# Kernel optimization log

Measured on AMD Instinct MI355X. Metric: run time of the kernel, lower is better.

Reference implementation:

```python
import jax, jax.numpy as jnp
import numpy as np

D_HEAD = 64
SCALE = 1.0 / (D_HEAD ** 0.5)
MASK_VALUE = -1e9


def setup_inputs() -> dict:
    key = jax.random.key(0)
    kq, kk, kv, km = jax.random.split(key, 4)
    B, H, S, D = 2, 12, 2048, D_HEAD
    Q = jax.random.normal(kq, (B, H, S, D), dtype=jnp.float32)
    K = jax.random.normal(kk, (B, H, S, D), dtype=jnp.float32)
    V = jax.random.normal(kv, (B, H, S, D), dtype=jnp.float32)
    attn_mask = jax.random.randint(km, (B, 1, S, S), 0, 2).astype(bool)
    return {"Q": Q, "K": K, "V": V, "attn_mask": attn_mask}


def reference(Q, K, V, attn_mask):
    # scores: [B,H,S,S]
    scores = jnp.einsum('bhqd,bhkd->bhqk', Q, K) * SCALE
    scores = jnp.where(attn_mask, MASK_VALUE, scores)
    attn_prob = jax.nn.softmax(scores, axis=-1)
    # dropout p=0.0 (eval mode) -> identity
    context = jnp.einsum('bhqk,bhkd->bhqd', attn_prob, V)
    return (context, attn_prob)
```

## Files before the change

### kernel.cpp

```cpp
#include <hip/hip_runtime.h>
#include <hip/hip_bf16.h>
#include <math.h>

#define B_SZ   2
#define NH     12
#define S_LEN  2048
#define D_HD   64
#define NQ_EL  ((size_t)B_SZ * NH * S_LEN * D_HD)

typedef __attribute__((ext_vector_type(8))) __bf16 bf16x8;
typedef __attribute__((ext_vector_type(4))) __bf16 bf16x4;
typedef __attribute__((ext_vector_type(4))) float  f32x4;
typedef __attribute__((ext_vector_type(4))) unsigned u32x4;

__device__ __forceinline__ int detect_mask_mode64(const void* mask) {
  const int lane = threadIdx.x & 63;
  unsigned v = ((const unsigned*)mask)[lane];
  if (__ballot(v <= 1u) == ~0ull) return 0;
  if (__ballot(v == 0u || v == 0x3f800000u) == ~0ull) return 2;
  unsigned h0 = v & 0xFFFFu, h1 = v >> 16;
  bool okb = (h0 == 0u || h0 == 0x3f80u) && (h1 == 0u || h1 == 0x3f80u);
  if (__ballot(okb) == ~0ull) return 3;
  return 1;
}

__device__ __forceinline__ bool mask_at(const void* mask, int mode, size_t idx) {
  if (mode == 0) return ((const int*)mask)[idx] != 0;
  if (mode == 1) return ((const unsigned char*)mask)[idx] != 0;
  if (mode == 2) return ((const float*)mask)[idx] != 0.0f;
  return ((const unsigned short*)mask)[idx] != 0;
}

__global__ __launch_bounds__(256)
void prep_kernel(const float* __restrict__ Q, const float* __restrict__ K,
                 const float* __restrict__ V, const void* __restrict__ mask,
                 unsigned* __restrict__ bits, __bf16* __restrict__ Qb,
                 __bf16* __restrict__ Kb, __bf16* __restrict__ VT) {
  const int blk = blockIdx.x;
  const int tid = threadIdx.x;
  if (blk < 512) {
    const int mode = detect_mask_mode64(mask);
    const int lane = tid & 63;
#pragma unroll 4
    for (int i = 0; i < 64; ++i) {
      const size_t idx = ((size_t)blk * 64 + i) * 256 + tid;
      const unsigned long long bal = __ballot(mask_at(mask, mode, idx));
      if (lane == 0)       bits[idx >> 5] = (unsigned)bal;
      else if (lane == 32) bits[idx >> 5] = (unsigned)(bal >> 32);
    }
  } else if (blk < 1536) {
    const bool isq = blk < 1024;
    const float* src = isq ? Q : K;
    __bf16* dst = isq ? Qb : Kb;
    const float scale = isq ? 0.125f : 1.0f;
    const size_t base = (size_t)(blk & 511) * 256 + tid;
#pragma unroll
    for (int i = 0; i < 6; ++i) {
      const size_t li = base + (size_t)i * 512 * 256;
      float4 a = ((const float4*)src)[li];
      __bf16 o0 = (__bf16)(a.x * scale), o1 = (__bf16)(a.y * scale);
      __bf16 o2 = (__bf16)(a.z * scale), o3 = (__bf16)(a.w * scale);
      ((ushort4*)dst)[li] = (ushort4){
          __builtin_bit_cast(unsigned short, o0), __builtin_bit_cast(unsigned short, o1),
          __builtin_bit_cast(unsigned short, o2), __builtin_bit_cast(unsigned short, o3)};
    }
  } else {
    __shared__ __align__(16) __bf16 tl[D_HD][72];
    const int t  = blk - 1536;
    const int bh = t >> 5;
    const int k0 = (t & 31) * 64;
#pragma unroll
    for (int i = 0; i < 4; ++i) {
      const int vi = i * 256 + tid;
      const int kk = vi >> 4, dv = (vi & 15) * 4;
      float4 f = *(const float4*)(V + ((size_t)bh * S_LEN + k0 + kk) * D_HD + dv);
      tl[dv + 0][kk] = (__bf16)f.x; tl[dv + 1][kk] = (__bf16)f.y;
      tl[dv + 2][kk] = (__bf16)f.z; tl[dv + 3][kk] = (__bf16)f.w;
    }
    __syncthreads();
#pragma unroll
    for (int half = 0; half < 2; ++half) {
      const int d = half * 32 + (tid >> 3);
      const int kc = (tid & 7) * 8;
      bf16x8 vv = *(const bf16x8*)&tl[d][kc];
      *(bf16x8*)(VT + ((size_t)bh * D_HD + d) * S_LEN + k0 + kc) = vv;
    }
  }
}

__device__ __forceinline__ bf16x8 ld8f(const float* p, float scale) {
  const float4 a = *(const float4*)p;
  const float4 b = *(const float4*)(p + 4);
  bf16x8 r;
  r[0] = (__bf16)(a.x * scale); r[1] = (__bf16)(a.y * scale);
  r[2] = (__bf16)(a.z * scale); r[3] = (__bf16)(a.w * scale);
  r[4] = (__bf16)(b.x * scale); r[5] = (__bf16)(b.y * scale);
  r[6] = (__bf16)(b.z * scale); r[7] = (__bf16)(b.w * scale);
  return r;
}

__device__ __forceinline__ float bflo(unsigned u) {
  return __builtin_bit_cast(float, u << 16);
}
__device__ __forceinline__ float bfhi(unsigned u) {
  return __builtin_bit_cast(float, u & 0xFFFF0000u);
}

__global__ __launch_bounds__(512, 4)
void attn_main(const __bf16* __restrict__ Qb, const __bf16* __restrict__ Kb,
               const __bf16* __restrict__ VT, const unsigned* __restrict__ mbits,
               float* __restrict__ out_ctx)
{
  float* out_p = out_ctx + NQ_EL;

  const int flat = blockIdx.x + blockIdx.y * gridDim.x;
  const int wf   = (flat & 7) * 384 + (flat >> 3);
  const int bh   = wf >> 7;
  const int qg   = wf & 127;
  const int b    = bh / NH;

  const int tid  = threadIdx.x;
  const int lane = tid & 63;
  const int w    = tid >> 6;
  const int qbase = qg * 16;
  const int col  = lane & 15;
  const int g    = lane >> 4;
  const int q    = qbase + col;
  const int k0   = w * 256;

  const size_t mbase = ((size_t)b * S_LEN + q) * (S_LEN / 32);
  const size_t khead = (size_t)bh * S_LEN;

  const size_t qoff = (khead + q) * D_HD + g * 8;
  const bf16x8 bq0 = *(const bf16x8*)(Qb + qoff);
  const bf16x8 bq1 = *(const bf16x8*)(Qb + qoff + 32);

  __shared__ float lsh[8][16];
  __shared__ float linv_s[16];
  __shared__ float csum[8][16][66];

  unsigned pe[8][4];
  float lsum = 0.f;

  bf16x8 nk0a, nk0b, nk1a, nk1b;
  {
    const size_t koff0 = (khead + k0 + col) * D_HD + g * 8;
    const size_t koff1 = (khead + k0 + 16 + col) * D_HD + g * 8;
    nk0a = *(const bf16x8*)(Kb + koff0);
    nk0b = *(const bf16x8*)(Kb + koff0 + 32);
    nk1a = *(const bf16x8*)(Kb + koff1);
    nk1b = *(const bf16x8*)(Kb + koff1 + 32);
  }
  unsigned nmw = mbits[mbase + (k0 >> 5)];

#pragma unroll
  for (int c = 0; c < 8; ++c) {
    const bf16x8 k0a = nk0a, k0b = nk0b, k1a = nk1a, k1b = nk1b;
    const unsigned mw = nmw;
    if (c < 7) {
      const int kn = k0 + (c + 1) * 32;
      const size_t koff0 = (khead + kn + col) * D_HD + g * 8;
      const size_t koff1 = (khead + kn + 16 + col) * D_HD + g * 8;
      nk0a = *(const bf16x8*)(Kb + koff0);
      nk0b = *(const bf16x8*)(Kb + koff0 + 32);
      nk1a = *(const bf16x8*)(Kb + koff1);
      nk1b = *(const bf16x8*)(Kb + koff1 + 32);
      nmw = mbits[mbase + (kn >> 5)];
    }
    float e[8];
    {
      f32x4 acc = {0.f, 0.f, 0.f, 0.f};
      acc = __builtin_amdgcn_mfma_f32_16x16x32_bf16(k0a, bq0, acc, 0, 0, 0);
      acc = __builtin_amdgcn_mfma_f32_16x16x32_bf16(k0b, bq1, acc, 0, 0, 0);
#pragma unroll
      for (int r = 0; r < 4; ++r) {
        const bool msk = (mw >> (g * 4 + r)) & 1;
        e[r] = msk ? 0.f : __expf(acc[r]);
        lsum += e[r];
      }
    }
    {
      f32x4 acc = {0.f, 0.f, 0.f, 0.f};
      acc = __builtin_amdgcn_mfma_f32_16x16x32_bf16(k1a, bq0, acc, 0, 0, 0);
      acc = __builtin_amdgcn_mfma_f32_16x16x32_bf16(k1b, bq1, acc, 0, 0, 0);
#pragma unroll
      for (int r = 0; r < 4; ++r) {
        const bool msk = (mw >> (16 + g * 4 + r)) & 1;
        e[4 + r] = msk ? 0.f : __expf(acc[r]);
        lsum += e[4 + r];
      }
    }
#pragma unroll
    for (int j = 0; j < 4; ++j) {
      unsigned lo = __builtin_bit_cast(unsigned short, (__bf16)e[2 * j]);
      unsigned hi = __builtin_bit_cast(unsigned short, (__bf16)e[2 * j + 1]);
      pe[c][j] = (hi << 16) | lo;
    }
  }
  lsum += __shfl_xor(lsum, 16);
  lsum += __shfl_xor(lsum, 32);
  if (lane < 16) lsh[w][col] = lsum;
  __syncthreads();
  {
    float tot = 0.f;
#pragma unroll
    for (int w8 = 0; w8 < 8; ++w8) tot += lsh[w8][col];
    if (w == 0 && lane < 16) linv_s[col] = 1.0f / tot;
  }
  const int Lr = lane >> 3;
  const int u  = lane & 7;
  float linv_t[2];
#pragma unroll
  for (int t = 0; t < 2; ++t) {
    float tot = 0.f;
#pragma unroll
    for (int w8 = 0; w8 < 8; ++w8) tot += lsh[w8][t * 8 + Lr];
    linv_t[t] = 1.0f / tot;
  }
  const int subg = u >> 2;

  f32x4 cacc[4];
#pragma unroll
  for (int dt = 0; dt < 4; dt++) cacc[dt] = (f32x4){0.f, 0.f, 0.f, 0.f};

  float* pblk = out_p + (size_t)bh * S_LEN * S_LEN + (size_t)qbase * S_LEN + k0;
  const __bf16* vbase = VT + (size_t)bh * D_HD * S_LEN;

#pragma unroll
  for (int c = 0; c < 8; ++c) {
    const int kc = k0 + c * 32;
    bf16x8 vf[4];
#pragma unroll
    for (int dt = 0; dt < 4; dt++) {
      const __bf16* vrow = vbase + (size_t)(dt * 16 + col) * S_LEN + kc;
      bf16x4 lo = *(const bf16x4*)(vrow + g * 4);
      bf16x4 hi = *(const bf16x4*)(vrow + 16 + g * 4);
      vf[dt] = __builtin_shufflevector(lo, hi, 0, 1, 2, 3, 4, 5, 6, 7);
    }
#pragma unroll
    for (int t = 0; t < 2; ++t) {
      const int src = 16 * (u & 3) + t * 8 + Lr;
      unsigned a0 = (unsigned)__shfl((int)pe[c][0], src);
      unsigned a1 = (unsigned)__shfl((int)pe[c][1], src);
      unsigned a2 = (unsigned)__shfl((int)pe[c][2], src);
      unsigned a3 = (unsigned)__shfl((int)pe[c][3], src);
      const unsigned lo = subg ? a2 : a0;
      const unsigned hi = subg ? a3 : a1;
      const float lv = linv_t[t];
      f32x4 st = {bflo(lo) * lv, bfhi(lo) * lv, bflo(hi) * lv, bfhi(hi) * lv};
      __builtin_nontemporal_store(
          st, (f32x4*)(pblk + (size_t)(t * 8 + Lr) * S_LEN + c * 32 + u * 4));
    }
    u32x4 w4 = {pe[c][0], pe[c][1], pe[c][2], pe[c][3]};
    bf16x8 pa = __builtin_bit_cast(bf16x8, w4);
#pragma unroll
    for (int dt = 0; dt < 4; dt++)
      cacc[dt] = __builtin_amdgcn_mfma_f32_16x16x32_bf16(pa, vf[dt], cacc[dt], 0, 0, 0);
  }

#pragma unroll
  for (int dt = 0; dt < 4; dt++)
#pragma unroll
    for (int r = 0; r < 4; r++)
      csum[w][g * 4 + r][dt * 16 + col] = cacc[dt][r];
  __syncthreads();
  {
    const int qo = tid >> 5;
    const int d0 = (tid * 2) & 63;
    float s0 = 0.f, s1 = 0.f;
#pragma unroll
    for (int w8 = 0; w8 < 8; ++w8) {
      s0 += csum[w8][qo][d0];
      s1 += csum[w8][qo][d0 + 1];
    }
    const float lv = linv_s[qo];
    float2 o = {s0 * lv, s1 * lv};
    *(float2*)(out_ctx + ((size_t)bh * S_LEN + qbase + qo) * D_HD + d0) = o;
  }
}

template<bool USE_BITS>
__global__ __launch_bounds__(512)
void attn_fb(const float* __restrict__ Qg, const float* __restrict__ Kg,
             const float* __restrict__ Vg, const void* __restrict__ mask,
             const unsigned* __restrict__ mbits, float* __restrict__ out_ctx)
{
  float* out_p = out_ctx + NQ_EL;
  const int flat = blockIdx.x + blockIdx.y * gridDim.x;
  const int wf   = (flat & 7) * 96 + (flat >> 3);
  const int qt = wf & 31, bh = wf >> 5, b = bh / NH;
  const int tid = threadIdx.x, lane = tid & 63, w = tid >> 6;
  const int qw = w & 3, kh = w >> 2;
  const int qbase = qt * 64 + qw * 16;
  const int col = lane & 15, g = lane >> 4;
  const int q = qbase + col;
  const int k0 = kh * (S_LEN / 2);
  int mmode = 0;
  if constexpr (!USE_BITS) mmode = detect_mask_mode64(mask);
  const size_t mrow  = (size_t)b * S_LEN * S_LEN;
  const size_t mbase = ((size_t)b * S_LEN + q) * (S_LEN / 32);
  const size_t qoff = ((size_t)bh * S_LEN + q) * D_HD + g * 8;
  const bf16x8 bq0 = ld8f(Qg + qoff, 0.125f);
  const bf16x8 bq1 = ld8f(Qg + qoff + 32, 0.125f);

  float lsum = 0.f;
  for (int kc = k0; kc < k0 + S_LEN / 2; kc += 32) {
    unsigned mw = 0;
    if constexpr (USE_BITS) mw = mbits[mbase + (kc >> 5)];
#pragma unroll
    for (int sub = 0; sub < 2; ++sub) {
      const int kb = kc + sub * 16;
      const size_t koff = ((size_t)bh * S_LEN + kb + col) * D_HD + g * 8;
      bf16x8 ak0 = ld8f(Kg + koff, 1.0f);
      bf16x8 ak1 = ld8f(Kg + koff + 32, 1.0f);
      f32x4 acc = {0.f, 0.f, 0.f, 0.f};
      acc = __builtin_amdgcn_mfma_f32_16x16x32_bf16(ak0, bq0, acc, 0, 0, 0);
      acc = __builtin_amdgcn_mfma_f32_16x16x32_bf16(ak1, bq1, acc, 0, 0, 0);
#pragma unroll
      for (int r = 0; r < 4; ++r) {
        bool msk;
        if constexpr (USE_BITS) msk = (mw >> (sub * 16 + g * 4 + r)) & 1;
        else msk = mask_at(mask, mmode, mrow + (size_t)q * S_LEN + kb + g * 4 + r);
        lsum += msk ? 0.f : __expf(acc[r]);
      }
    }
  }
  lsum += __shfl_xor(lsum, 16);
  lsum += __shfl_xor(lsum, 32);
  __shared__ float lsh[8][16];
  __shared__ float csum[4][16][66];
  if (lane < 16) lsh[w][col] = lsum;
  __syncthreads();
  const float inv_l = 1.0f / (lsum + lsh[w ^ 4][col]);

  f32x4 cacc[4];
#pragma unroll
  for (int dt = 0; dt < 4; dt++) cacc[dt] = (f32x4){0.f, 0.f, 0.f, 0.f};
  float* prow = out_p + (size_t)bh * S_LEN * S_LEN + (size_t)q * S_LEN;

  for (int it = 0; it < S_LEN / 64; ++it) {
    const int kc = k0 + it * 32;
    unsigned mw = 0;
    if constexpr (USE_BITS) mw = mbits[mbase + (kc >> 5)];
    float p[8];
#pragma unroll
    for (int sub = 0; sub < 2; ++sub) {
      const int kb = kc + sub * 16;
      const size_t koff = ((size_t)bh * S_LEN + kb + col) * D_HD + g * 8;
      bf16x8 ak0 = ld8f(Kg + koff, 1.0f);
      bf16x8 ak1 = ld8f(Kg + koff + 32, 1.0f);
      f32x4 acc = {0.f, 0.f, 0.f, 0.f};
      acc = __builtin_amdgcn_mfma_f32_16x16x32_bf16(ak0, bq0, acc, 0, 0, 0);
      acc = __builtin_amdgcn_mfma_f32_16x16x32_bf16(ak1, bq1, acc, 0, 0, 0);
#pragma unroll
      for (int r = 0; r < 4; ++r) {
        bool msk;
        if constexpr (USE_BITS) msk = (mw >> (sub * 16 + g * 4 + r)) & 1;
        else msk = mask_at(mask, mmode, mrow + (size_t)q * S_LEN + kb + g * 4 + r);
        p[sub * 4 + r] = msk ? 0.f : __expf(acc[r]) * inv_l;
      }
      float4 st = {p[sub * 4 + 0], p[sub * 4 + 1], p[sub * 4 + 2], p[sub * 4 + 3]};
      *(float4*)(prow + kb + g * 4) = st;
    }
    bf16x8 pa;
#pragma unroll
    for (int e = 0; e < 8; e++) pa[e] = (__bf16)p[e];
#pragma unroll
    for (int dt = 0; dt < 4; dt++) {
      bf16x8 vf;
#pragma unroll
      for (int e = 0; e < 8; e++) {
        const int kidx = kc + (e >> 2) * 16 + g * 4 + (e & 3);
        vf[e] = (__bf16)Vg[((size_t)bh * S_LEN + kidx) * D_HD + dt * 16 + col];
      }
      cacc[dt] = __builtin_amdgcn_mfma_f32_16x16x32_bf16(pa, vf, cacc[dt], 0, 0, 0);
    }
  }
  if (kh == 1) {
#pragma unroll
    for (int dt = 0; dt < 4; dt++)
#pragma unroll
      for (int r = 0; r < 4; r++)
        csum[qw][g * 4 + r][dt * 16 + col] = cacc[dt][r];
  }
  __syncthreads();
  if (kh == 0) {
#pragma unroll
    for (int dt = 0; dt < 4; dt++)
#pragma unroll
      for (int r = 0; r < 4; r++)
        out_ctx[((size_t)bh * S_LEN + qbase + g * 4 + r) * D_HD + dt * 16 + col] =
            cacc[dt][r] + csum[qw][g * 4 + r][dt * 16 + col];
  }
}

__global__ __launch_bounds__(256)
void build_bits_kernel(const void* __restrict__ mask, unsigned* __restrict__ bits) {
  const int mode = detect_mask_mode64(mask);
  const size_t i = (size_t)blockIdx.x * 256 + threadIdx.x;
  const unsigned long long bal = __ballot(mask_at(mask, mode, i));
  const int lane = threadIdx.x & 63;
  if (lane == 0)       bits[i >> 5] = (unsigned)bal;
  else if (lane == 32) bits[i >> 5] = (unsigned)(bal >> 32);
}

extern "C" void kernel_launch(void* const* d_in, const int* in_sizes, int n_in,
                              void* d_out, int out_size, void* d_ws, size_t ws_size,
                              hipStream_t stream) {
  const float* Q = (const float*)d_in[0];
  const float* K = (const float*)d_in[1];
  const float* V = (const float*)d_in[2];
  const void* mask = d_in[3];
  float* out = (float*)d_out;

  const size_t mask_elems = (size_t)B_SZ * S_LEN * S_LEN;
  const size_t off_bits = 256;
  const size_t off_q  = off_bits + mask_elems / 8;
  const size_t off_k  = off_q + NQ_EL * 2;
  const size_t off_vt = off_k + NQ_EL * 2;
  const size_t need   = off_vt + NQ_EL * 2;

  if (ws_size >= need) {
    unsigned* bits = (unsigned*)((char*)d_ws + off_bits);
    __bf16* Qb = (__bf16*)((char*)d_ws + off_q);
    __bf16* Kb = (__bf16*)((char*)d_ws + off_k);
    __bf16* VT = (__bf16*)((char*)d_ws + off_vt);
    prep_kernel<<<2304, 256, 0, stream>>>(Q, K, V, mask, bits, Qb, Kb, VT);
    dim3 grid(128, 24);
    attn_main<<<grid, 512, 0, stream>>>(Qb, Kb, VT, bits, out);
  } else if (ws_size >= off_q) {
    unsigned* bits = (unsigned*)((char*)d_ws + off_bits);
    build_bits_kernel<<<(unsigned)(mask_elems / 256), 256, 0, stream>>>(mask, bits);
    dim3 gfb(S_LEN / 64, B_SZ * NH);
    attn_fb<true><<<gfb, 512, 0, stream>>>(Q, K, V, mask, bits, out);
  } else {
    dim3 gfb(S_LEN / 64, B_SZ * NH);
    attn_fb<false><<<gfb, 512, 0, stream>>>(Q, K, V, mask, nullptr, out);
  }
}
```

Measured before the change: 313.6 us.

## Split attention into compute pass and separate probability normalization kernel

The main attention kernel now writes unnormalized bf16 exponentials and per-row inverse sums to workspace, computes the context, and leaves probability output to a new streaming normalization kernel. The aim is to decouple the large fp32 probability write from the MFMA compute kernel and give it fully coalesced row-contiguous stores. This adds a large intermediate write and read through workspace, and it runs only when the workspace is big enough; otherwise the old monolithic kernel is used.

```diff
diff --git a/kernel.cpp b/kernel.cpp
--- a/kernel.cpp
+++ b/kernel.cpp
@@ -7,6 +7,7 @@
 #define S_LEN  2048
 #define D_HD   64
 #define NQ_EL  ((size_t)B_SZ * NH * S_LEN * D_HD)
+#define NROWS  ((size_t)B_SZ * NH * S_LEN)
 
 typedef __attribute__((ext_vector_type(8))) __bf16 bf16x8;
 typedef __attribute__((ext_vector_type(4))) __bf16 bf16x4;
@@ -107,12 +108,11 @@
 }
 
 __global__ __launch_bounds__(512, 4)
-void attn_main(const __bf16* __restrict__ Qb, const __bf16* __restrict__ Kb,
-               const __bf16* __restrict__ VT, const unsigned* __restrict__ mbits,
-               float* __restrict__ out_ctx)
+void attn_compute(const __bf16* __restrict__ Qb, const __bf16* __restrict__ Kb,
+                  const __bf16* __restrict__ VT, const unsigned* __restrict__ mbits,
+                  float* __restrict__ out_ctx, unsigned short* __restrict__ ebuf,
+                  float* __restrict__ linvg)
 {
-  float* out_p = out_ctx + NQ_EL;
-
   const int flat = blockIdx.x + blockIdx.y * gridDim.x;
   const int wf   = (flat & 7) * 384 + (flat >> 3);
   const int bh   = wf >> 7;
@@ -196,6 +196,14 @@
       unsigned hi = __builtin_bit_cast(unsigned short, (__bf16)e[2 * j + 1]);
       pe[c][j] = (hi << 16) | lo;
     }
+    const int kc = k0 + c * 32;
+    unsigned long long v01 = (unsigned long long)pe[c][0] |
+                             ((unsigned long long)pe[c][1] << 32);
+    unsigned long long v23 = (unsigned long long)pe[c][2] |
+                             ((unsigned long long)pe[c][3] << 32);
+    unsigned short* erow = ebuf + (khead + q) * S_LEN;
+    *(unsigned long long*)(erow + kc + g * 4)      = v01;
+    *(unsigned long long*)(erow + kc + 16 + g * 4) = v23;
   }
   lsum += __shfl_xor(lsum, 16);
   lsum += __shfl_xor(lsum, 32);
@@ -205,6 +213,142 @@
     float tot = 0.f;
 #pragma unroll
     for (int w8 = 0; w8 < 8; ++w8) tot += lsh[w8][col];
+    if (w == 0 && lane < 16) {
+      const float lv = 1.0f / tot;
+      linv_s[col] = lv;
+      linvg[khead + q] = lv;
+    }
+  }
+
+  f32x4 cacc[4];
+#pragma unroll
+  for (int dt = 0; dt < 4; dt++) cacc[dt] = (f32x4){0.f, 0.f, 0.f, 0.f};
+  const __bf16* vbase = VT + (size_t)bh * D_HD * S_LEN;
+
+#pragma unroll
+  for (int c = 0; c < 8; ++c) {
+    const int kc = k0 + c * 32;
+    u32x4 w4 = {pe[c][0], pe[c][1], pe[c][2], pe[c][3]};
+    bf16x8 pa = __builtin_bit_cast(bf16x8, w4);
+#pragma unroll
+    for (int dt = 0; dt < 4; dt++) {
+      const __bf16* vrow = vbase + (size_t)(dt * 16 + col) * S_LEN + kc;
+      bf16x4 lo = *(const bf16x4*)(vrow + g * 4);
+      bf16x4 hi = *(const bf16x4*)(vrow + 16 + g * 4);
+      bf16x8 vf = __builtin_shufflevector(lo, hi, 0, 1, 2, 3, 4, 5, 6, 7);
+      cacc[dt] = __builtin_amdgcn_mfma_f32_16x16x32_bf16(pa, vf, cacc[dt], 0, 0, 0);
+    }
+  }
+
+#pragma unroll
+  for (int dt = 0; dt < 4; dt++)
+#pragma unroll
+    for (int r = 0; r < 4; r++)
+      csum[w][g * 4 + r][dt * 16 + col] = cacc[dt][r];
+  __syncthreads();
+  {
+    const int qo = tid >> 5;
+    const int d0 = (tid * 2) & 63;
+    float s0 = 0.f, s1 = 0.f;
+#pragma unroll
+    for (int w8 = 0; w8 < 8; ++w8) {
+      s0 += csum[w8][qo][d0];
+      s1 += csum[w8][qo][d0 + 1];
+    }
+    const float lv = linv_s[qo];
+    float2 o = {s0 * lv, s1 * lv};
+    *(float2*)(out_ctx + ((size_t)bh * S_LEN + qbase + qo) * D_HD + d0) = o;
+  }
+}
+
+__global__ __launch_bounds__(256)
+void norm_kernel(const unsigned short* __restrict__ ebuf,
+                 const float* __restrict__ linvg, float* __restrict__ out_p)
+{
+  const int tid = threadIdx.x;
+#pragma unroll
+  for (int i = 0; i < 16; ++i) {
+    const size_t row = (size_t)blockIdx.x * 16 + i;
+    const float lv = linvg[row];
+    const unsigned short* erow = ebuf + row * S_LEN;
+    float* prow = out_p + row * S_LEN;
+#pragma unroll
+    for (int s = 0; s < 2; ++s) {
+      const int col = s * 1024 + tid * 4;
+      const unsigned long long v = *(const unsigned long long*)(erow + col);
+      const unsigned u0 = (unsigned)v, u1 = (unsigned)(v >> 32);
+      f32x4 st = {bflo(u0) * lv, bfhi(u0) * lv, bflo(u1) * lv, bfhi(u1) * lv};
+      *(f32x4*)(prow + col) = st;
+    }
+  }
+}
+
+__global__ __launch_bounds__(512, 4)
+void attn_mono(const __bf16* __restrict__ Qb, const __bf16* __restrict__ Kb,
+               const __bf16* __restrict__ VT, const unsigned* __restrict__ mbits,
+               float* __restrict__ out_ctx)
+{
+  float* out_p = out_ctx + NQ_EL;
+  const int flat = blockIdx.x + blockIdx.y * gridDim.x;
+  const int wf   = (flat & 7) * 384 + (flat >> 3);
+  const int bh   = wf >> 7;
+  const int qg   = wf & 127;
+  const int b    = bh / NH;
+  const int tid  = threadIdx.x;
+  const int lane = tid & 63;
+  const int w    = tid >> 6;
+  const int qbase = qg * 16;
+  const int col  = lane & 15;
+  const int g    = lane >> 4;
+  const int q    = qbase + col;
+  const int k0   = w * 256;
+  const size_t mbase = ((size_t)b * S_LEN + q) * (S_LEN / 32);
+  const size_t khead = (size_t)bh * S_LEN;
+  const size_t qoff = (khead + q) * D_HD + g * 8;
+  const bf16x8 bq0 = *(const bf16x8*)(Qb + qoff);
+  const bf16x8 bq1 = *(const bf16x8*)(Qb + qoff + 32);
+  __shared__ float lsh[8][16];
+  __shared__ float linv_s[16];
+  __shared__ float csum[8][16][66];
+  unsigned pe[8][4];
+  float lsum = 0.f;
+#pragma unroll
+  for (int c = 0; c < 8; ++c) {
+    const int kc = k0 + c * 32;
+    const unsigned mw = mbits[mbase + (kc >> 5)];
+    float e[8];
+#pragma unroll
+    for (int sub = 0; sub < 2; ++sub) {
+      const int kb = kc + sub * 16;
+      const size_t koff = (khead + kb + col) * D_HD + g * 8;
+      bf16x8 ak0 = *(const bf16x8*)(Kb + koff);
+      bf16x8 ak1 = *(const bf16x8*)(Kb + koff + 32);
+      f32x4 acc = {0.f, 0.f, 0.f, 0.f};
+      acc = __builtin_amdgcn_mfma_f32_16x16x32_bf16(ak0, bq0, acc, 0, 0, 0);
+      acc = __builtin_amdgcn_mfma_f32_16x16x32_bf16(ak1, bq1, acc, 0, 0, 0);
+#pragma unroll
+      for (int r = 0; r < 4; ++r) {
+        const bool msk = (mw >> (sub * 16 + g * 4 + r)) & 1;
+        float ev = msk ? 0.f : __expf(acc[r]);
+        e[sub * 4 + r] = ev;
+        lsum += ev;
+      }
+    }
+#pragma unroll
+    for (int j = 0; j < 4; ++j) {
+      unsigned lo = __builtin_bit_cast(unsigned short, (__bf16)e[2 * j]);
+      unsigned hi = __builtin_bit_cast(unsigned short, (__bf16)e[2 * j + 1]);
+      pe[c][j] = (hi << 16) | lo;
+    }
+  }
+  lsum += __shfl_xor(lsum, 16);
+  lsum += __shfl_xor(lsum, 32);
+  if (lane < 16) lsh[w][col] = lsum;
+  __syncthreads();
+  {
+    float tot = 0.f;
+#pragma unroll
+    for (int w8 = 0; w8 < 8; ++w8) tot += lsh[w8][col];
     if (w == 0 && lane < 16) linv_s[col] = 1.0f / tot;
   }
   const int Lr = lane >> 3;
@@ -218,14 +362,11 @@
     linv_t[t] = 1.0f / tot;
   }
   const int subg = u >> 2;
-
   f32x4 cacc[4];
 #pragma unroll
   for (int dt = 0; dt < 4; dt++) cacc[dt] = (f32x4){0.f, 0.f, 0.f, 0.f};
-
   float* pblk = out_p + (size_t)bh * S_LEN * S_LEN + (size_t)qbase * S_LEN + k0;
   const __bf16* vbase = VT + (size_t)bh * D_HD * S_LEN;
-
 #pragma unroll
   for (int c = 0; c < 8; ++c) {
     const int kc = k0 + c * 32;
@@ -257,7 +398,6 @@
     for (int dt = 0; dt < 4; dt++)
       cacc[dt] = __builtin_amdgcn_mfma_f32_16x16x32_bf16(pa, vf[dt], cacc[dt], 0, 0, 0);
   }
-
 #pragma unroll
   for (int dt = 0; dt < 4; dt++)
 #pragma unroll
@@ -412,22 +552,37 @@
   const float* V = (const float*)d_in[2];
   const void* mask = d_in[3];
   float* out = (float*)d_out;
+  float* out_p = out + NQ_EL;
 
   const size_t mask_elems = (size_t)B_SZ * S_LEN * S_LEN;
   const size_t off_bits = 256;
-  const size_t off_q  = off_bits + mask_elems / 8;
-  const size_t off_k  = off_q + NQ_EL * 2;
-  const size_t off_vt = off_k + NQ_EL * 2;
-  const size_t need   = off_vt + NQ_EL * 2;
-
-  if (ws_size >= need) {
+  const size_t off_q    = off_bits + mask_elems / 8;
+  const size_t off_k    = off_q + NQ_EL * 2;
+  const size_t off_vt   = off_k + NQ_EL * 2;
+  const size_t need_r12 = off_vt + NQ_EL * 2;
+  const size_t off_linv = need_r12;
+  const size_t off_e    = off_linv + NROWS * 4;
+  const size_t need_spl = off_e + mask_elems * 2;
+
+  if (ws_size >= need_spl) {
+    unsigned* bits = (unsigned*)((char*)d_ws + off_bits);
+    __bf16* Qb = (__bf16*)((char*)d_ws + off_q);
+    __bf16* Kb = (__bf16*)((char*)d_ws + off_k);
+    __bf16* VT = (__bf16*)((char*)d_ws + off_vt);
+    float* linvg = (float*)((char*)d_ws + off_linv);
+    unsigned short* ebuf = (unsigned short*)((char*)d_ws + off_e);
+    prep_kernel<<<2304, 256, 0, stream>>>(Q, K, V, mask, bits, Qb, Kb, VT);
+    dim3 grid(128, 24);
+    attn_compute<<<grid, 512, 0, stream>>>(Qb, Kb, VT, bits, out, ebuf, linvg);
+    norm_kernel<<<3072, 256, 0, stream>>>(ebuf, linvg, out_p);
+  } else if (ws_size >= need_r12) {
     unsigned* bits = (unsigned*)((char*)d_ws + off_bits);
     __bf16* Qb = (__bf16*)((char*)d_ws + off_q);
     __bf16* Kb = (__bf16*)((char*)d_ws + off_k);
     __bf16* VT = (__bf16*)((char*)d_ws + off_vt);
     prep_kernel<<<2304, 256, 0, stream>>>(Q, K, V, mask, bits, Qb, Kb, VT);
     dim3 grid(128, 24);
-    attn_main<<<grid, 512, 0, stream>>>(Qb, Kb, VT, bits, out);
+    attn_mono<<<grid, 512, 0, stream>>>(Qb, Kb, VT, bits, out);
   } else if (ws_size >= off_q) {
     unsigned* bits = (unsigned*)((char*)d_ws + off_bits);
     build_bits_kernel<<<(unsigned)(mask_elems / 256), 256, 0, stream>>>(mask, bits);
```

Measured after the change: 470.0 us. 1.5x slower.
